# Kernel tuning notes

Measured on AMD Instinct MI355X. Metric: run time of the kernel, lower is better.

The kernel has to match this reference:

```python
import jax, jax.numpy as jnp
import numpy as np


def setup_inputs() -> dict:
    key = jax.random.key(0)
    k1, k2 = jax.random.split(key)
    B, F = 512, 1024
    K, D = 100, 5
    inputs = jax.random.normal(k1, (B, F), dtype=jnp.float32)
    T = jax.random.normal(k2, (F, K * D), dtype=jnp.float32) * 0.05  # random_normal init
    return {"inputs": inputs, "T": T}


def reference(inputs, T):
    NUM_KERNELS, DIM_PER_KERNEL = 100, 5
    B = inputs.shape[0]
    # project: [B, F] @ [F, K*D] -> [B, K, D]
    x = (inputs @ T).reshape(B, NUM_KERNELS, DIM_PER_KERNEL)
    # pairwise L1 over D: abs_diffs[i, k, j] = sum_d |x[i,k,d] - x[j,k,d]|
    # diffs: [B, K, D, B]
    diffs = x[:, :, :, None] - jnp.transpose(x, (1, 2, 0))[None, :, :, :]
    abs_diffs = jnp.sum(jnp.abs(diffs), axis=2)  # [B, K, B]
    # sum over other-batch axis (includes self term exp(0)=1, as in original)
    minibatch_features = jnp.sum(jnp.exp(-abs_diffs), axis=2)  # [B, K]
    return minibatch_features
```

## Files before the change

kernel.cpp:

```cpp
#include <hip/hip_runtime.h>


#define BB 512
#define FF 1024
#define KK 100
#define KD 500
#define KDP 512
#define SPLITS 8
#define FN (FF / SPLITS)
#define STEPS (FN / 16)
#define LOG2E 1.4426950408889634f

__global__ __launch_bounds__(256, 2) void kA(
    const float* __restrict__ in, const float* __restrict__ T,
    float* __restrict__ xpT)
{
    __shared__ __align__(16) float smem[2112];
    float (*Ads)[68] = (float(*)[68])smem;
    float (*Bds)[64] = (float(*)[64])(smem + 1088);

    const int b = blockIdx.x;
    const int t = threadIdx.x;
    const int i0  = (b & 7) * 64;
    const int kd0 = ((b >> 3) & 7) * 64;
    const int s   = b >> 6;
    const int tk  = t & 15;
    const int ti  = t >> 4;

    float acc[4][4];
    #pragma unroll
    for (int r = 0; r < 4; ++r)
        #pragma unroll
        for (int c = 0; c < 4; ++c) acc[r][c] = 0.f;

    const int ia  = t >> 2;
    const int fqa = t & 3;
    const int kb  = t & 63;
    const int frb = t >> 6;
    const int kbc = min(kd0 + kb, KD - 1);

    const float* inb = in + (size_t)(i0 + ia) * FF + s * FN;
    const float* Tb  = T + (size_t)(s * FN) * KD + kbc;

    float4 av = *(const float4*)&inb[fqa * 4];
    float bv0 = Tb[(size_t)(frb * 4 + 0) * KD];
    float bv1 = Tb[(size_t)(frb * 4 + 1) * KD];
    float bv2 = Tb[(size_t)(frb * 4 + 2) * KD];
    float bv3 = Tb[(size_t)(frb * 4 + 3) * KD];

    for (int step = 0; step < STEPS; ++step) {
        Ads[fqa * 4 + 0][ia] = av.x;
        Ads[fqa * 4 + 1][ia] = av.y;
        Ads[fqa * 4 + 2][ia] = av.z;
        Ads[fqa * 4 + 3][ia] = av.w;
        Bds[frb * 4 + 0][kb] = bv0;
        Bds[frb * 4 + 1][kb] = bv1;
        Bds[frb * 4 + 2][kb] = bv2;
        Bds[frb * 4 + 3][kb] = bv3;
        __syncthreads();

        if (step + 1 < STEPS) {
            const int fo = (step + 1) * 16;
            av  = *(const float4*)&inb[fo + fqa * 4];
            bv0 = Tb[(size_t)(fo + frb * 4 + 0) * KD];
            bv1 = Tb[(size_t)(fo + frb * 4 + 1) * KD];
            bv2 = Tb[(size_t)(fo + frb * 4 + 2) * KD];
            bv3 = Tb[(size_t)(fo + frb * 4 + 3) * KD];
        }

        #pragma unroll
        for (int f = 0; f < 16; ++f) {
            float4 a  = *(const float4*)&Ads[f][ti * 4];
            float4 bq = *(const float4*)&Bds[f][tk * 4];
            float ar[4] = {a.x, a.y, a.z, a.w};
            float br[4] = {bq.x, bq.y, bq.z, bq.w};
            #pragma unroll
            for (int r = 0; r < 4; ++r)
                #pragma unroll
                for (int c = 0; c < 4; ++c)
                    acc[r][c] = fmaf(ar[r], br[c], acc[r][c]);
        }
        __syncthreads();
    }

    #pragma unroll
    for (int c = 0; c < 4; ++c) {
        float4 v = {acc[0][c], acc[1][c], acc[2][c], acc[3][c]};
        *(float4*)&xpT[((size_t)s * KDP + kd0 + tk * 4 + c) * BB + i0 + ti * 4] = v;
    }
}

__global__ __launch_bounds__(512) void pair2k(
    const float* __restrict__ xpT, float* __restrict__ out)
{
    const int kp = blockIdx.x;
    const int ip = blockIdx.y;
    const int t  = threadIdx.x;
    const int lane = t & 63;
    const int w    = t >> 6;

    __shared__ float xs[BB][12];
    __shared__ float ps[8][128][2];

    const int kb0 = kp * 10;
    #pragma unroll
    for (int c = 0; c < 10; ++c) {
        float v = 0.f;
        #pragma unroll
        for (int s = 0; s < SPLITS; ++s)
            v += xpT[((size_t)s * KDP + kb0 + c) * BB + t];
        xs[t][c] = LOG2E * v;
    }
    __syncthreads();

    float xi[2][10];
    #pragma unroll
    for (int r = 0; r < 2; ++r) {
        const int i = ip * 128 + r * 64 + lane;
        #pragma unroll
        for (int c = 0; c < 10; ++c) xi[r][c] = xs[i][c];
    }

    float a00 = 0.f, a01 = 0.f, a10 = 0.f, a11 = 0.f;
    const int j0 = w << 6;
    #pragma unroll 2
    for (int jj = 0; jj < 64; ++jj) {
        const int j = j0 + jj;
        float4 xjA = *(const float4*)&xs[j][0];
        float4 xjB = *(const float4*)&xs[j][4];
        float2 xjC = *(const float2*)&xs[j][8];
        {
            float aa = (fabsf(xi[0][0] - xjA.x) + fabsf(xi[0][1] - xjA.y))
                     + (fabsf(xi[0][2] - xjA.z) + fabsf(xi[0][3] - xjA.w))
                     + fabsf(xi[0][4] - xjB.x);
            float bb = (fabsf(xi[0][5] - xjB.y) + fabsf(xi[0][6] - xjB.z))
                     + (fabsf(xi[0][7] - xjB.w) + fabsf(xi[0][8] - xjC.x))
                     + fabsf(xi[0][9] - xjC.y);
            a00 += __builtin_amdgcn_exp2f(-aa);
            a01 += __builtin_amdgcn_exp2f(-bb);
        }
        {
            float aa = (fabsf(xi[1][0] - xjA.x) + fabsf(xi[1][1] - xjA.y))
                     + (fabsf(xi[1][2] - xjA.z) + fabsf(xi[1][3] - xjA.w))
                     + fabsf(xi[1][4] - xjB.x);
            float bb = (fabsf(xi[1][5] - xjB.y) + fabsf(xi[1][6] - xjB.z))
                     + (fabsf(xi[1][7] - xjB.w) + fabsf(xi[1][8] - xjC.x))
                     + fabsf(xi[1][9] - xjC.y);
            a10 += __builtin_amdgcn_exp2f(-aa);
            a11 += __builtin_amdgcn_exp2f(-bb);
        }
    }

    ps[w][lane][0]      = a00;
    ps[w][lane][1]      = a01;
    ps[w][lane + 64][0] = a10;
    ps[w][lane + 64][1] = a11;
    __syncthreads();

    if (t < 256) {
        const int il = t >> 1;
        const int kk = t & 1;
        float v = 0.f;
        #pragma unroll
        for (int q = 0; q < 8; ++q) v += ps[q][il][kk];
        out[(size_t)(ip * 128 + il) * KK + kp * 2 + kk] = v;
    }
}

__global__ __launch_bounds__(1024, 1) void mbd_fused(
    const float* __restrict__ in, const float* __restrict__ T, float* __restrict__ out)
{
    const int k = blockIdx.x;
    const int t = threadIdx.x;
    const int i = t & (BB - 1);
    const int h = t >> 9;

    __shared__ float xk[1024][8];

    float a0 = 0.f, a1 = 0.f, a2 = 0.f, a3 = 0.f, a4 = 0.f;
    const float4* inrow = (const float4*)(in + (size_t)i * FF + (size_t)h * 512);
    const float* Tk = T + 5 * k + (size_t)h * 512 * KD;

    for (int ff = 0; ff < 512; ff += 4) {
        float4 v = inrow[ff >> 2];
        const float* tp = Tk + (size_t)ff * KD;
        a0 = fmaf(v.x, tp[0], a0); a1 = fmaf(v.x, tp[1], a1); a2 = fmaf(v.x, tp[2], a2);
        a3 = fmaf(v.x, tp[3], a3); a4 = fmaf(v.x, tp[4], a4); tp += KD;
        a0 = fmaf(v.y, tp[0], a0); a1 = fmaf(v.y, tp[1], a1); a2 = fmaf(v.y, tp[2], a2);
        a3 = fmaf(v.y, tp[3], a3); a4 = fmaf(v.y, tp[4], a4); tp += KD;
        a0 = fmaf(v.z, tp[0], a0); a1 = fmaf(v.z, tp[1], a1); a2 = fmaf(v.z, tp[2], a2);
        a3 = fmaf(v.z, tp[3], a3); a4 = fmaf(v.z, tp[4], a4); tp += KD;
        a0 = fmaf(v.w, tp[0], a0); a1 = fmaf(v.w, tp[1], a1); a2 = fmaf(v.w, tp[2], a2);
        a3 = fmaf(v.w, tp[3], a3); a4 = fmaf(v.w, tp[4], a4);
    }
    xk[t][0] = a0; xk[t][1] = a1; xk[t][2] = a2; xk[t][3] = a3; xk[t][4] = a4;
    __syncthreads();
    if (t < BB) {
        xk[t][0] += xk[t + BB][0]; xk[t][1] += xk[t + BB][1]; xk[t][2] += xk[t + BB][2];
        xk[t][3] += xk[t + BB][3]; xk[t][4] += xk[t + BB][4];
    }
    __syncthreads();

    const int jg = t >> 9;
    const float4 xiv = *(const float4*)&xk[i][0];
    const float xi4 = xk[i][4];
    float s0 = 0.f;
    const int j0 = jg << 8;
    for (int jj = 0; jj < 256; ++jj) {
        const int j = j0 + jj;
        float4 xj = *(const float4*)&xk[j][0];
        float xj4 = xk[j][4];
        float aa = (fabsf(xiv.x - xj.x) + fabsf(xiv.y - xj.y))
                 + (fabsf(xiv.z - xj.z) + fabsf(xiv.w - xj.w)) + fabsf(xi4 - xj4);
        s0 += __builtin_amdgcn_exp2f(-1.4426950408889634f * aa);
    }
    xk[BB + i][jg] = s0;
    __syncthreads();
    if (t < BB)
        out[(size_t)t * KK + k] = xk[BB + t][0] + xk[BB + t][1];
}

extern "C" void kernel_launch(void* const* d_in, const int* in_sizes, int n_in,
                              void* d_out, int out_size, void* d_ws, size_t ws_size,
                              hipStream_t stream) {
    const float* in = (const float*)d_in[0];
    const float* T  = (const float*)d_in[1];
    float* out = (float*)d_out;

    const size_t xpT_bytes = (size_t)SPLITS * KDP * BB * sizeof(float);

    if (ws_size < xpT_bytes) {
        mbd_fused<<<KK, 1024, 0, stream>>>(in, T, out);
        return;
    }

    float* xpT = (float*)d_ws;

    kA<<<512, 256, 0, stream>>>(in, T, xpT);

    dim3 g2(KK / 2, 4);
    pair2k<<<g2, 512, 0, stream>>>(xpT, out);
}
```

Measured before the change: 37.61 us.

## Split pairwise stage into reduce kernel plus j-split pair kernel with atomics

Adds a separate kernel that reduces the split-K partial projections once into a padded row layout, so the pairwise kernel no longer repeats that reduction for every i-block. The pairwise kernel now reads j rows straight from global memory with uniform block indices instead of staging through shared memory. It splits the j range across a third grid dimension and accumulates into the output with atomic adds, which doubles the number of blocks. In exchange it adds a memset and an extra kernel launch, plus atomic traffic and float summation order that can vary between runs.

```diff
diff --git a/kernel.cpp b/kernel.cpp
--- a/kernel.cpp
+++ b/kernel.cpp
@@ -10,6 +10,8 @@
 #define FN (FF / SPLITS)
 #define STEPS (FN / 16)
 #define LOG2E 1.4426950408889634f
+#define NKP 50
+#define XQROW 16
 
 __global__ __launch_bounds__(256, 2) void kA(
     const float* __restrict__ in, const float* __restrict__ T,
@@ -90,67 +92,90 @@
     }
 }
 
-__global__ __launch_bounds__(512) void pair2k(
-    const float* __restrict__ xpT, float* __restrict__ out)
-{
-    const int kp = blockIdx.x;
-    const int ip = blockIdx.y;
+__global__ __launch_bounds__(256) void kB2(
+    const float* __restrict__ xpT, float* __restrict__ xqT)
+{
+    const int e  = blockIdx.x * 256 + threadIdx.x;
+    const int kp = e >> 9;
+    const int i  = e & 511;
+
+    float v[10];
+    #pragma unroll
+    for (int c = 0; c < 10; ++c) {
+        float a = 0.f;
+        #pragma unroll
+        for (int s = 0; s < SPLITS; ++s)
+            a += xpT[((size_t)s * KDP + kp * 10 + c) * BB + i];
+        v[c] = LOG2E * a;
+    }
+
+    float* row = xqT + ((size_t)kp * BB + i) * XQROW;
+    float4 w0 = {v[0], v[1], v[2], v[3]};
+    float4 w1 = {v[4], v[5], v[6], v[7]};
+    float2 w2 = {v[8], v[9]};
+    *(float4*)&row[0] = w0;
+    *(float4*)&row[4] = w1;
+    *(float2*)&row[8] = w2;
+}
+
+__global__ __launch_bounds__(256) void pairS(
+    const float* __restrict__ xqT, float* __restrict__ out)
+{
+    const int kp = __builtin_amdgcn_readfirstlane(blockIdx.x);
+    const int ip = __builtin_amdgcn_readfirstlane(blockIdx.y);
+    const int jp = __builtin_amdgcn_readfirstlane(blockIdx.z);
     const int t  = threadIdx.x;
     const int lane = t & 63;
     const int w    = t >> 6;
 
-    __shared__ float xs[BB][12];
-    __shared__ float ps[8][128][2];
-
-    const int kb0 = kp * 10;
-    #pragma unroll
-    for (int c = 0; c < 10; ++c) {
-        float v = 0.f;
-        #pragma unroll
-        for (int s = 0; s < SPLITS; ++s)
-            v += xpT[((size_t)s * KDP + kb0 + c) * BB + t];
-        xs[t][c] = LOG2E * v;
-    }
-    __syncthreads();
+    const float* __restrict__ xk = xqT + (size_t)kp * BB * XQROW;
 
     float xi[2][10];
     #pragma unroll
     for (int r = 0; r < 2; ++r) {
-        const int i = ip * 128 + r * 64 + lane;
-        #pragma unroll
-        for (int c = 0; c < 10; ++c) xi[r][c] = xs[i][c];
+        const float* row = xk + (size_t)(ip * 128 + r * 64 + lane) * XQROW;
+        float4 a = *(const float4*)&row[0];
+        float4 b = *(const float4*)&row[4];
+        float2 c = *(const float2*)&row[8];
+        xi[r][0] = a.x; xi[r][1] = a.y; xi[r][2] = a.z; xi[r][3] = a.w;
+        xi[r][4] = b.x; xi[r][5] = b.y; xi[r][6] = b.z; xi[r][7] = b.w;
+        xi[r][8] = c.x; xi[r][9] = c.y;
     }
 
     float a00 = 0.f, a01 = 0.f, a10 = 0.f, a11 = 0.f;
-    const int j0 = w << 6;
+    const int j0 = jp * 256 + w * 64;
+    const float* __restrict__ jrow = xk + (size_t)j0 * XQROW;
+
     #pragma unroll 2
     for (int jj = 0; jj < 64; ++jj) {
-        const int j = j0 + jj;
-        float4 xjA = *(const float4*)&xs[j][0];
-        float4 xjB = *(const float4*)&xs[j][4];
-        float2 xjC = *(const float2*)&xs[j][8];
+        const float* row = jrow + (size_t)jj * XQROW;
+        const float b0 = row[0], b1 = row[1], b2 = row[2], b3 = row[3];
+        const float b4 = row[4], b5 = row[5], b6 = row[6], b7 = row[7];
+        const float b8 = row[8], b9 = row[9];
+
         {
-            float aa = (fabsf(xi[0][0] - xjA.x) + fabsf(xi[0][1] - xjA.y))
-                     + (fabsf(xi[0][2] - xjA.z) + fabsf(xi[0][3] - xjA.w))
-                     + fabsf(xi[0][4] - xjB.x);
-            float bb = (fabsf(xi[0][5] - xjB.y) + fabsf(xi[0][6] - xjB.z))
-                     + (fabsf(xi[0][7] - xjB.w) + fabsf(xi[0][8] - xjC.x))
-                     + fabsf(xi[0][9] - xjC.y);
+            float aa = (fabsf(xi[0][0] - b0) + fabsf(xi[0][1] - b1))
+                     + (fabsf(xi[0][2] - b2) + fabsf(xi[0][3] - b3))
+                     + fabsf(xi[0][4] - b4);
+            float bb = (fabsf(xi[0][5] - b5) + fabsf(xi[0][6] - b6))
+                     + (fabsf(xi[0][7] - b7) + fabsf(xi[0][8] - b8))
+                     + fabsf(xi[0][9] - b9);
             a00 += __builtin_amdgcn_exp2f(-aa);
             a01 += __builtin_amdgcn_exp2f(-bb);
         }
         {
-            float aa = (fabsf(xi[1][0] - xjA.x) + fabsf(xi[1][1] - xjA.y))
-                     + (fabsf(xi[1][2] - xjA.z) + fabsf(xi[1][3] - xjA.w))
-                     + fabsf(xi[1][4] - xjB.x);
-            float bb = (fabsf(xi[1][5] - xjB.y) + fabsf(xi[1][6] - xjB.z))
-                     + (fabsf(xi[1][7] - xjB.w) + fabsf(xi[1][8] - xjC.x))
-                     + fabsf(xi[1][9] - xjC.y);
+            float aa = (fabsf(xi[1][0] - b0) + fabsf(xi[1][1] - b1))
+                     + (fabsf(xi[1][2] - b2) + fabsf(xi[1][3] - b3))
+                     + fabsf(xi[1][4] - b4);
+            float bb = (fabsf(xi[1][5] - b5) + fabsf(xi[1][6] - b6))
+                     + (fabsf(xi[1][7] - b7) + fabsf(xi[1][8] - b8))
+                     + fabsf(xi[1][9] - b9);
             a10 += __builtin_amdgcn_exp2f(-aa);
             a11 += __builtin_amdgcn_exp2f(-bb);
         }
     }
 
+    __shared__ float ps[4][128][2];
     ps[w][lane][0]      = a00;
     ps[w][lane][1]      = a01;
     ps[w][lane + 64][0] = a10;
@@ -160,10 +185,9 @@
     if (t < 256) {
         const int il = t >> 1;
         const int kk = t & 1;
-        float v = 0.f;
-        #pragma unroll
-        for (int q = 0; q < 8; ++q) v += ps[q][il][kk];
-        out[(size_t)(ip * 128 + il) * KK + kp * 2 + kk] = v;
+        float v = (ps[0][il][kk] + ps[1][il][kk])
+                + (ps[2][il][kk] + ps[3][il][kk]);
+        unsafeAtomicAdd(&out[(size_t)(ip * 128 + il) * KK + kp * 2 + kk], v);
     }
 }
 
@@ -228,16 +252,21 @@
     float* out = (float*)d_out;
 
     const size_t xpT_bytes = (size_t)SPLITS * KDP * BB * sizeof(float);
-
-    if (ws_size < xpT_bytes) {
+    const size_t xq_bytes  = (size_t)NKP * BB * XQROW * sizeof(float);
+
+    if (ws_size < xpT_bytes + xq_bytes) {
         mbd_fused<<<KK, 1024, 0, stream>>>(in, T, out);
         return;
     }
 
     float* xpT = (float*)d_ws;
+    float* xqT = (float*)((char*)d_ws + xpT_bytes);
+
+    hipMemsetAsync(out, 0, (size_t)BB * KK * sizeof(float), stream);
 
     kA<<<512, 256, 0, stream>>>(in, T, xpT);
-
-    dim3 g2(KK / 2, 4);
-    pair2k<<<g2, 512, 0, stream>>>(xpT, out);
-}
+    kB2<<<100, 256, 0, stream>>>(xpT, xqT);
+
+    dim3 g3(NKP, 4, 2);
+    pairS<<<g3, 256, 0, stream>>>(xqT, out);
+}
```

New measurement: 53.81 us. +43.1%, slower.
